# Kernel tuning notes

Hardware: AMD Instinct MI355X
Metric: run time of the kernel (lower is better)

## Reference

```python
import jax, jax.numpy as jnp
import numpy as np

N, K, DIN = 2, 2048, 1024
H, DOUT = 16, 64


def setup_inputs() -> dict:
    key = jax.random.key(0)
    ks = jax.random.split(key, 12)
    c_qk = float(np.sqrt(6.0 / (DIN + DOUT)))  # per-head q/k init scale
    c_v = c_qk  # dim_q == dim_v == DOUT here
    u = lambda k, shape, c: jax.random.uniform(k, shape, jnp.float32, -c, c)
    inp = {
        "query": jax.random.normal(ks[0], (N, K, DIN), jnp.float32),
        "key": jax.random.normal(ks[1], (N, K, DIN), jnp.float32),
        "value": jax.random.normal(ks[2], (N, K, DIN), jnp.float32),
        "mask": jax.random.randint(ks[3], (N, K, K), 0, 2) > 0,  # bool (N,K,K)
        # stacked per-head projection weights: (H, DIN, DOUT), biases (H, DOUT)
        "Wq": u(ks[4], (H, DIN, DOUT), c_qk),
        "bq": u(ks[5], (H, DOUT), c_qk),
        "Wk": u(ks[6], (H, DIN, DOUT), c_qk),
        "bk": u(ks[7], (H, DOUT), c_qk),
        "Wv": u(ks[8], (H, DIN, DOUT), c_v),
        "bv": u(ks[9], (H, DOUT), c_v),
        # output projection: (H*DOUT, DIN)
        "Wp": u(ks[10], (H * DOUT, DIN), c_qk),
        "bp": u(ks[11], (DIN,), c_qk),
    }
    return inp


def reference(query, key, value, mask, Wq, bq, Wk, bk, Wv, bv, Wp, bp):
    # Per-head projections, batched over heads: (N,K,DIN) x (H,DIN,DOUT) -> (N,H,K,DOUT)
    q = jnp.einsum("nkm,hmd->nhkd", query, Wq) + bq[None, :, None, :]
    k = jnp.einsum("nkm,hmd->nhkd", key, Wk) + bk[None, :, None, :]
    v = jnp.einsum("nkm,hmd->nhkd", value, Wv) + bv[None, :, None, :]
    # scaled dot-product scores: (N,H,K,K), scaled by sqrt(per-head dim)
    scores = jnp.einsum("nhkd,nhld->nhkl", q, k) / jnp.sqrt(jnp.asarray(DOUT, q.dtype))
    scores = jnp.where(mask[:, None, :, :], jnp.asarray(-1e9, scores.dtype), scores)
    w = jax.nn.softmax(scores, axis=-1)
    y = jnp.einsum("nhkl,nhld->nhkd", w, v)  # (N,H,K,DOUT)
    # concat heads along feature dim (head order matches torch cat over head list)
    y = jnp.transpose(y, (0, 2, 1, 3)).reshape(N, K, H * DOUT)
    return y @ Wp + bp
```

## Files before the change

kernel.cpp:

```cpp
#include <hip/hip_runtime.h>
#include <hip/hip_bf16.h>
#include <stdint.h>

typedef __attribute__((ext_vector_type(8))) __bf16 bf16x8;
typedef __attribute__((ext_vector_type(2))) __bf16 bf16x2;
typedef __attribute__((ext_vector_type(4))) float floatx4;

#define NB 2
#define SEQ 2048
#define DIN 1024
#define NH 16
#define DH 64
#define DMODEL 1024
#define BQ 128
#define BK 64
#define PAD 72
#define QSCALE 0.18033688011112042f

__device__ __forceinline__ float bf2f(unsigned short u) {
    return __uint_as_float(((unsigned)u) << 16);
}
__device__ __forceinline__ unsigned short f2bf(float f) {
    unsigned u = __float_as_uint(f);
    unsigned r = (u + 0x7FFFu + ((u >> 16) & 1u)) >> 16;
    return (unsigned short)r;
}
__device__ __forceinline__ float ldin(const void* p, size_t idx, int isbf) {
    return isbf ? bf2f(((const unsigned short*)p)[idx]) : ((const float*)p)[idx];
}

__device__ __forceinline__ void gl_lds16(const void* g, void* l) {
    __builtin_amdgcn_global_load_lds(
        reinterpret_cast<__attribute__((address_space(1))) unsigned int*>(
            reinterpret_cast<uintptr_t>(g)),
        reinterpret_cast<__attribute__((address_space(3))) unsigned int*>(
            reinterpret_cast<uintptr_t>(l)),
        16, 0, 0);
}

__device__ __forceinline__ int wave_is_bf16(const void* p) {
    unsigned short u = ((const unsigned short*)p)[2 * (threadIdx.x & 63)];
    int e = (u >> 7) & 0xFF;
    int sane = (u == 0 || (e > 100 && e < 140)) ? 1 : 0;
    return __popcll(__ballot(sane)) >= 32;
}
__device__ __forceinline__ int wave_mask_is_int(const void* p) {
    int v = ((const int*)p)[threadIdx.x & 63];
    int zo = (v == 0 || v == 1) ? 1 : 0;
    return __popcll(__ballot(zo)) >= 48;
}

__global__ __launch_bounds__(256) void prep(
    const void* __restrict__ q, const void* __restrict__ k, const void* __restrict__ v,
    const void* __restrict__ mask,
    const void* __restrict__ wq, const void* __restrict__ wk,
    const void* __restrict__ wv, const void* __restrict__ wp,
    unsigned short* __restrict__ a0, unsigned short* __restrict__ a1,
    unsigned short* __restrict__ a2,
    unsigned short* __restrict__ t0, unsigned short* __restrict__ t1,
    unsigned short* __restrict__ t2, unsigned short* __restrict__ t3,
    unsigned int* __restrict__ mbits)
{
    __shared__ float xls[64][68];
    const int b = blockIdx.x;
    const int tid = threadIdx.x;
    if (b < 12288) {
        int z = b >> 12, blk = b & 4095;
        const void* src = (z == 0) ? q : (z == 1) ? k : v;
        unsigned short* dst = (z == 0) ? a0 : (z == 1) ? a1 : a2;
        int isbf = wave_is_bf16(src);
        size_t i = ((size_t)blk * 256 + tid) * 4;
        if (isbf) {
            *(ushort4*)&dst[i] = *(const ushort4*)((const unsigned short*)src + i);
        } else {
            float4 f = *(const float4*)((const float*)src + i);
            ushort4 o;
            o.x = f2bf(f.x); o.y = f2bf(f.y); o.z = f2bf(f.z); o.w = f2bf(f.w);
            *(ushort4*)&dst[i] = o;
        }
    } else if (b < 13312) {
        int blk = b - 12288;
        int w = blk * 256 + tid;
        int is_int = wave_mask_is_int(mask);
        unsigned bits = 0;
        if (is_int) {
            const int4* p = (const int4*)mask + (size_t)w * 8;
#pragma unroll
            for (int g = 0; g < 8; ++g) {
                int4 vv = p[g];
                bits |= (unsigned)(vv.x != 0) << (g * 4 + 0);
                bits |= (unsigned)(vv.y != 0) << (g * 4 + 1);
                bits |= (unsigned)(vv.z != 0) << (g * 4 + 2);
                bits |= (unsigned)(vv.w != 0) << (g * 4 + 3);
            }
        } else {
            const uint4* p = (const uint4*)mask + (size_t)w * 2;
#pragma unroll
            for (int g = 0; g < 2; ++g) {
                uint4 vv = p[g];
                unsigned ws4[4] = {vv.x, vv.y, vv.z, vv.w};
#pragma unroll
                for (int c = 0; c < 4; ++c)
#pragma unroll
                    for (int bb = 0; bb < 4; ++bb)
                        bits |= (unsigned)(((ws4[c] >> (8 * bb)) & 0xFFu) != 0)
                                << (g * 16 + c * 4 + bb);
            }
        }
        mbits[w] = bits;
    } else {
        int zb = b - 13312;
        int z = zb >> 8, t = zb & 255;
        const void* src = (z == 0) ? wq : (z == 1) ? wk : (z == 2) ? wv : wp;
        unsigned short* dst = (z == 0) ? t0 : (z == 1) ? t1 : (z == 2) ? t2 : t3;
        int isbf = wave_is_bf16(src);
        int r = tid >> 2, cs = (tid & 3) * 16;
        if (z < 3) {
            int h = t >> 4, m0 = (t & 15) * 64;
#pragma unroll
            for (int j = 0; j < 16; ++j)
                xls[r][cs + j] = ldin(src, (size_t)h * 65536 + (size_t)(m0 + r) * 64 + cs + j, isbf);
            __syncthreads();
            int d2 = tid >> 2, ms = (tid & 3) * 16;
            size_t orow = (size_t)(h * 64 + d2) * 1024 + m0 + ms;
#pragma unroll
            for (int g = 0; g < 4; ++g) {
                ushort4 o;
                o.x = f2bf(xls[ms + g * 4 + 0][d2]);
                o.y = f2bf(xls[ms + g * 4 + 1][d2]);
                o.z = f2bf(xls[ms + g * 4 + 2][d2]);
                o.w = f2bf(xls[ms + g * 4 + 3][d2]);
                *(ushort4*)&dst[orow + g * 4] = o;
            }
        } else {
            int m0 = (t >> 4) * 64, c0 = (t & 15) * 64;
#pragma unroll
            for (int j = 0; j < 16; ++j)
                xls[r][cs + j] = ldin(src, (size_t)(m0 + r) * 1024 + c0 + cs + j, isbf);
            __syncthreads();
            int d2 = tid >> 2, ms = (tid & 3) * 16;
            size_t orow = (size_t)(c0 + d2) * 1024 + m0 + ms;
#pragma unroll
            for (int g = 0; g < 4; ++g) {
                ushort4 o;
                o.x = f2bf(xls[ms + g * 4 + 0][d2]);
                o.y = f2bf(xls[ms + g * 4 + 1][d2]);
                o.z = f2bf(xls[ms + g * 4 + 2][d2]);
                o.w = f2bf(xls[ms + g * 4 + 3][d2]);
                *(ushort4*)&dst[orow + g * 4] = o;
            }
        }
    }
}

__global__ __launch_bounds__(256) void expand_mask(
    const unsigned int* __restrict__ mbits, unsigned short* __restrict__ m16)
{
    int gid = blockIdx.x * 256 + threadIdx.x;
    unsigned w = mbits[gid];
    unsigned wrd[16];
#pragma unroll
    for (int i = 0; i < 16; ++i) {
        unsigned lo = ((w >> (2 * i)) & 1u) - 1u;
        unsigned hi = ((w >> (2 * i + 1)) & 1u) - 1u;
        wrd[i] = (lo & 0xFFFFu) | (hi << 16);
    }
    uint4* dst = (uint4*)&m16[(size_t)gid * 32];
#pragma unroll
    for (int g = 0; g < 4; ++g) dst[g] = *(uint4*)&wrd[g * 4];
}

__global__ __launch_bounds__(256) void gemm_mfma(
    const unsigned short* __restrict__ A0, const unsigned short* __restrict__ A1,
    const unsigned short* __restrict__ A2,
    const unsigned short* __restrict__ B0, const unsigned short* __restrict__ B1,
    const unsigned short* __restrict__ B2,
    const void* __restrict__ bias0, const void* __restrict__ bias1,
    const void* __restrict__ bias2,
    void* __restrict__ C0, void* __restrict__ C1, void* __restrict__ C2,
    int mode0)
{
    const int z = blockIdx.z;
    const unsigned short* A  = (z == 0) ? A0 : (z == 1) ? A1 : A2;
    const unsigned short* BT = (z == 0) ? B0 : (z == 1) ? B1 : B2;
    const void* bias = (z == 0) ? bias0 : (z == 1) ? bias1 : bias2;
    void* C = (z == 0) ? C0 : (z == 1) ? C1 : C2;
    const int mode = mode0 + z;
    const int isbf = wave_is_bf16(bias);
    const float scl = (mode == 0) ? QSCALE : 1.0f;

    const int n0  = blockIdx.x * 128;
    const int m0g = blockIdx.y * 128;
    const int tid = threadIdx.x;
    const int wave = tid >> 6, lane = tid & 63;
    const int l16 = lane & 15, quad = lane >> 4;
    const int wm = wave & 1, wn = wave >> 1;

    __shared__ __align__(16) unsigned short smem[17408];
    unsigned short* As = smem;
    unsigned short* Bs = smem + 8192;

    floatx4 acc[4][4];
#pragma unroll
    for (int mt = 0; mt < 4; ++mt)
#pragma unroll
        for (int nt = 0; nt < 4; ++nt) acc[mt][nt] = floatx4{0.f, 0.f, 0.f, 0.f};

    const int lrow8 = lane >> 3;
    const int lseg  = (lane & 7) * 8;

    for (int kk = 0; kk < 1024; kk += 64) {
#pragma unroll
        for (int j = 0; j < 4; ++j) {
            int row0 = wave * 8 + j * 32;
            gl_lds16(&A[(size_t)(m0g + row0 + lrow8) * 1024 + kk + lseg], &As[row0 * 64]);
            gl_lds16(&BT[(size_t)(n0 + row0 + lrow8) * 1024 + kk + lseg], &Bs[row0 * 64]);
        }
        __syncthreads();
#pragma unroll
        for (int ks = 0; ks < 2; ++ks) {
            bf16x8 af[4], bf[4];
#pragma unroll
            for (int mt = 0; mt < 4; ++mt)
                af[mt] = *(const bf16x8*)&As[(wm * 64 + mt * 16 + l16) * 64 + ks * 32 + quad * 8];
#pragma unroll
            for (int nt = 0; nt < 4; ++nt)
                bf[nt] = *(const bf16x8*)&Bs[(wn * 64 + nt * 16 + l16) * 64 + ks * 32 + quad * 8];
#pragma unroll
            for (int mt = 0; mt < 4; ++mt)
#pragma unroll
                for (int nt = 0; nt < 4; ++nt)
                    acc[mt][nt] = __builtin_amdgcn_mfma_f32_16x16x32_bf16(af[mt], bf[nt], acc[mt][nt], 0, 0, 0);
        }
        __syncthreads();
    }

    float bv4[4];
#pragma unroll
    for (int nt = 0; nt < 4; ++nt)
        bv4[nt] = ldin(bias, n0 + wn * 64 + nt * 16 + l16, isbf);

    if (mode <= 1) {
        unsigned short* O = (unsigned short*)C;
#pragma unroll
        for (int mt = 0; mt < 4; ++mt)
#pragma unroll
            for (int reg = 0; reg < 4; ++reg) {
                int row = m0g + wm * 64 + mt * 16 + quad * 4 + reg;
                int nb = row >> 11, kq = row & (SEQ - 1);
#pragma unroll
                for (int nt = 0; nt < 4; ++nt) {
                    int c = n0 + wn * 64 + nt * 16 + l16;
                    int h = c >> 6, d = c & 63;
                    O[(((size_t)nb * NH + h) * SEQ + kq) * DH + d] =
                        f2bf((acc[mt][nt][reg] + bv4[nt]) * scl);
                }
            }
    } else if (mode == 2) {
#pragma unroll
        for (int mt = 0; mt < 4; ++mt)
#pragma unroll
            for (int nt = 0; nt < 4; ++nt)
#pragma unroll
                for (int reg = 0; reg < 4; ++reg) {
                    int m_l = wm * 64 + mt * 16 + quad * 4 + reg;
                    int c_l = wn * 64 + nt * 16 + l16;
                    smem[c_l * 136 + m_l] = f2bf(acc[mt][nt][reg] + bv4[nt]);
                }
        __syncthreads();
        unsigned short* O = (unsigned short*)C;
        int nb = m0g >> 11;
        int kq0 = m0g & (SEQ - 1);
#pragma unroll
        for (int j = 0; j < 8; ++j) {
            int i = tid + j * 256;
            int c_l = i >> 4, m8 = (i & 15) * 8;
            int cg = n0 + c_l, h = cg >> 6, d = cg & 63;
            *(bf16x8*)&O[(((size_t)nb * NH + h) * DH + d) * SEQ + kq0 + m8] =
                *(const bf16x8*)&smem[c_l * 136 + m8];
        }
    } else {
        unsigned short* Ob = (unsigned short*)C;
        float* Of = (float*)C;
#pragma unroll
        for (int mt = 0; mt < 4; ++mt)
#pragma unroll
            for (int reg = 0; reg < 4; ++reg) {
                int row = m0g + wm * 64 + mt * 16 + quad * 4 + reg;
#pragma unroll
                for (int nt = 0; nt < 4; ++nt) {
                    int c = n0 + wn * 64 + nt * 16 + l16;
                    float v = acc[mt][nt][reg] + bv4[nt];
                    if (isbf) Ob[(size_t)row * DMODEL + c] = f2bf(v);
                    else      Of[(size_t)row * DMODEL + c] = v;
                }
            }
    }
}

__global__ __launch_bounds__(256, 2) void attn_mfma(
    const unsigned short* __restrict__ qws, const unsigned short* __restrict__ kws,
    const unsigned short* __restrict__ vtws, const unsigned short* __restrict__ m16,
    unsigned short* __restrict__ yws)
{
    const int qt   = blockIdx.x;
    const int h    = blockIdx.y;
    const int n    = blockIdx.z;
    const int tid  = threadIdx.x;
    const int wave = tid >> 6;
    const int lane = tid & 63;
    const int l16  = lane & 15;
    const int quad = lane >> 4;

    __shared__ __align__(16) unsigned short Ks[2][BK * DH];
    __shared__ __align__(16) unsigned short VTs[2][DH * BK];
    __shared__ __align__(16) unsigned short Ps[4][32 * PAD];

    const size_t base_nh = ((size_t)n * NH + h) * SEQ * DH;
    const size_t base_vt = ((size_t)n * NH + h) * DH * SEQ;
    const int q0 = qt * BQ;

    const unsigned short* mrl0;
    const unsigned short* mrl1;
    bf16x8 af[2][2];
    {
        int qr0 = q0 + wave * 32 + l16;
        int qr1 = qr0 + 16;
        mrl0 = m16 + ((size_t)n * SEQ + qr0) * SEQ;
        mrl1 = m16 + ((size_t)n * SEQ + qr1) * SEQ;
        const unsigned short* qp0 = qws + base_nh + (size_t)qr0 * DH + quad * 8;
        const unsigned short* qp1 = qws + base_nh + (size_t)qr1 * DH + quad * 8;
        af[0][0] = *(const bf16x8*)qp0;
        af[0][1] = *(const bf16x8*)(qp0 + 32);
        af[1][0] = *(const bf16x8*)qp1;
        af[1][1] = *(const bf16x8*)(qp1 + 32);
    }

    const int srow8  = lane >> 3;
    const int schunk = ((lane & 7) ^ srow8) * 8;
    const int swz = l16 & 7;
    int koff[2], voff[2];
#pragma unroll
    for (int ks = 0; ks < 2; ++ks) {
        koff[ks] = l16 * DH + (((ks * 4 + quad) ^ swz) * 8);
        voff[ks] = l16 * BK + (((ks * 4 + quad) ^ swz) * 8);
    }

    bf16x8 vones;
#pragma unroll
    for (int j = 0; j < 8; ++j) vones[j] = (__bf16)1.0f;

#pragma unroll
    for (int j = 0; j < 2; ++j) {
        int rl = wave * 16 + j * 8;
        gl_lds16(&kws[base_nh + (size_t)(rl + srow8) * DH + schunk], &Ks[0][rl * DH]);
        gl_lds16(&vtws[base_vt + (size_t)(rl + srow8) * SEQ + schunk], &VTs[0][rl * BK]);
    }

    floatx4 O[2][4];
#pragma unroll
    for (int g = 0; g < 2; ++g)
#pragma unroll
        for (int dt = 0; dt < 4; ++dt) O[g][dt] = floatx4{0.f, 0.f, 0.f, 0.f};
    floatx4 Lacc[2];
    Lacc[0] = floatx4{0.f, 0.f, 0.f, 0.f};
    Lacc[1] = floatx4{0.f, 0.f, 0.f, 0.f};

    __syncthreads();

    for (int it = 0; it < SEQ / BK; ++it) {
        const int cur = it & 1, nxt = cur ^ 1;
        const bool has_next = (it + 1) < (SEQ / BK);
        const int j0 = it * BK;
        const int j0n = j0 + BK;

        if (has_next) {
#pragma unroll
            for (int j = 0; j < 2; ++j) {
                int rl = wave * 16 + j * 8;
                gl_lds16(&kws[base_nh + (size_t)(j0n + rl + srow8) * DH + schunk], &Ks[nxt][rl * DH]);
                gl_lds16(&vtws[base_vt + (size_t)(rl + srow8) * SEQ + j0n + schunk], &VTs[nxt][rl * BK]);
            }
        }

        uint2 mm[2][4];
#pragma unroll
        for (int nt = 0; nt < 4; ++nt) {
            mm[0][nt] = *(const uint2*)&mrl0[j0 + nt * 16 + quad * 4];
            mm[1][nt] = *(const uint2*)&mrl1[j0 + nt * 16 + quad * 4];
        }

        bf16x8 bfK[4][2];
#pragma unroll
        for (int nt = 0; nt < 4; ++nt)
#pragma unroll
            for (int ks = 0; ks < 2; ++ks)
                bfK[nt][ks] = *(const bf16x8*)&Ks[cur][nt * 16 * DH + koff[ks]];

        float St[2][4][4];
#pragma unroll
        for (int nt = 0; nt < 4; ++nt) {
#pragma unroll
            for (int g = 0; g < 2; ++g) {
                floatx4 c = {0.f, 0.f, 0.f, 0.f};
                c = __builtin_amdgcn_mfma_f32_16x16x32_bf16(bfK[nt][0], af[g][0], c, 0, 0, 0);
                c = __builtin_amdgcn_mfma_f32_16x16x32_bf16(bfK[nt][1], af[g][1], c, 0, 0, 0);
                St[g][nt][0] = c[0]; St[g][nt][1] = c[1];
                St[g][nt][2] = c[2]; St[g][nt][3] = c[3];
            }
        }

#pragma unroll
        for (int g = 0; g < 2; ++g)
#pragma unroll
            for (int nt = 0; nt < 4; ++nt) {
                bf16x2 e01, e23;
                e01[0] = (__bf16)__builtin_amdgcn_exp2f(St[g][nt][0]);
                e01[1] = (__bf16)__builtin_amdgcn_exp2f(St[g][nt][1]);
                e23[0] = (__bf16)__builtin_amdgcn_exp2f(St[g][nt][2]);
                e23[1] = (__bf16)__builtin_amdgcn_exp2f(St[g][nt][3]);
                uint2 pk;
                pk.x = (*(unsigned*)&e01) & mm[g][nt].x;
                pk.y = (*(unsigned*)&e23) & mm[g][nt].y;
                *(uint2*)&Ps[wave][(g * 16 + l16) * PAD + nt * 16 + quad * 4] = pk;
            }

        bf16x8 pa[2][2], vb[4][2];
#pragma unroll
        for (int g = 0; g < 2; ++g)
#pragma unroll
            for (int ks = 0; ks < 2; ++ks)
                pa[g][ks] = *(const bf16x8*)&Ps[wave][(g * 16 + l16) * PAD + ks * 32 + quad * 8];
#pragma unroll
        for (int dt = 0; dt < 4; ++dt)
#pragma unroll
            for (int ks = 0; ks < 2; ++ks)
                vb[dt][ks] = *(const bf16x8*)&VTs[cur][dt * 16 * BK + voff[ks]];

        Lacc[0] = __builtin_amdgcn_mfma_f32_16x16x32_bf16(pa[0][0], vones, Lacc[0], 0, 0, 0);
        Lacc[1] = __builtin_amdgcn_mfma_f32_16x16x32_bf16(pa[1][0], vones, Lacc[1], 0, 0, 0);
        Lacc[0] = __builtin_amdgcn_mfma_f32_16x16x32_bf16(pa[0][1], vones, Lacc[0], 0, 0, 0);
        Lacc[1] = __builtin_amdgcn_mfma_f32_16x16x32_bf16(pa[1][1], vones, Lacc[1], 0, 0, 0);
#pragma unroll
        for (int dt = 0; dt < 4; ++dt) {
#pragma unroll
            for (int g = 0; g < 2; ++g) {
                O[g][dt] = __builtin_amdgcn_mfma_f32_16x16x32_bf16(pa[g][0], vb[dt][0], O[g][dt], 0, 0, 0);
                O[g][dt] = __builtin_amdgcn_mfma_f32_16x16x32_bf16(pa[g][1], vb[dt][1], O[g][dt], 0, 0, 0);
            }
        }

        __syncthreads();
    }

#pragma unroll
    for (int g = 0; g < 2; ++g)
#pragma unroll
        for (int r = 0; r < 4; ++r) {
            float lr = Lacc[g][r];
            float inv = (lr > 0.f) ? 1.f / lr : 0.f;
            int row = q0 + wave * 32 + g * 16 + quad * 4 + r;
#pragma unroll
            for (int dt = 0; dt < 4; ++dt) {
                int col = h * DH + dt * 16 + l16;
                yws[((size_t)n * SEQ + row) * DMODEL + col] = f2bf(O[g][dt][r] * inv);
            }
        }
}

extern "C" void kernel_launch(void* const* d_in, const int* in_sizes, int n_in,
                              void* d_out, int out_size, void* d_ws, size_t ws_size,
                              hipStream_t stream) {
    const void* query = d_in[0];
    const void* key_  = d_in[1];
    const void* value = d_in[2];
    const void* mask  = d_in[3];
    const void* Wq = d_in[4];
    const void* bq = d_in[5];
    const void* Wk = d_in[6];
    const void* bk = d_in[7];
    const void* Wv = d_in[8];
    const void* bv = d_in[9];
    const void* Wp = d_in[10];
    const void* bp = d_in[11];

    const size_t per = (size_t)NB * NH * SEQ * DH;
    unsigned short* us = (unsigned short*)d_ws;
    unsigned short* qws  = us;
    unsigned short* kws  = us + per;
    unsigned short* vtws = us + 2 * per;
    unsigned short* abf0 = us + 3 * per;
    unsigned short* abf1 = us + 4 * per;
    unsigned short* abf2 = us + 5 * per;
    unsigned short* wt0  = us + 6 * per;
    unsigned short* wt1  = wt0 + 1048576;
    unsigned short* wt2  = wt1 + 1048576;
    unsigned short* wt3  = wt2 + 1048576;
    unsigned int* mbits  = (unsigned int*)(wt3 + 1048576);
    unsigned short* yws = abf0;
    unsigned short* mask16 = abf1;

    prep<<<dim3(14336), 256, 0, stream>>>(query, key_, value, mask,
                                          Wq, Wk, Wv, Wp,
                                          abf0, abf1, abf2,
                                          wt0, wt1, wt2, wt3, mbits);
    gemm_mfma<<<dim3(8, 32, 3), 256, 0, stream>>>(abf0, abf1, abf2, wt0, wt1, wt2,
                                                  bq, bk, bv, qws, kws, vtws, 0);
    expand_mask<<<dim3(1024), 256, 0, stream>>>(mbits, mask16);
    attn_mfma<<<dim3(SEQ / BQ, NH, NB), 256, 0, stream>>>(qws, kws, vtws, mask16, yws);
    gemm_mfma<<<dim3(8, 32, 1), 256, 0, stream>>>(yws, yws, yws, wt3, wt3, wt3,
                                                  bp, bp, bp, d_out, d_out, d_out, 3);
}
```

Before: 310.8 us.

## Read packed mask bits directly in attention and remap blocks per XCD

```diff
diff --git a/kernel.cpp b/kernel.cpp
--- a/kernel.cpp
+++ b/kernel.cpp
@@ -153,23 +153,6 @@
     }
 }
 
-__global__ __launch_bounds__(256) void expand_mask(
-    const unsigned int* __restrict__ mbits, unsigned short* __restrict__ m16)
-{
-    int gid = blockIdx.x * 256 + threadIdx.x;
-    unsigned w = mbits[gid];
-    unsigned wrd[16];
-#pragma unroll
-    for (int i = 0; i < 16; ++i) {
-        unsigned lo = ((w >> (2 * i)) & 1u) - 1u;
-        unsigned hi = ((w >> (2 * i + 1)) & 1u) - 1u;
-        wrd[i] = (lo & 0xFFFFu) | (hi << 16);
-    }
-    uint4* dst = (uint4*)&m16[(size_t)gid * 32];
-#pragma unroll
-    for (int g = 0; g < 4; ++g) dst[g] = *(uint4*)&wrd[g * 4];
-}
-
 __global__ __launch_bounds__(256) void gemm_mfma(
     const unsigned short* __restrict__ A0, const unsigned short* __restrict__ A1,
     const unsigned short* __restrict__ A2,
@@ -300,12 +283,16 @@
 
 __global__ __launch_bounds__(256, 2) void attn_mfma(
     const unsigned short* __restrict__ qws, const unsigned short* __restrict__ kws,
-    const unsigned short* __restrict__ vtws, const unsigned short* __restrict__ m16,
+    const unsigned short* __restrict__ vtws, const unsigned int* __restrict__ mbits,
     unsigned short* __restrict__ yws)
 {
-    const int qt   = blockIdx.x;
-    const int h    = blockIdx.y;
-    const int n    = blockIdx.z;
+    const int linear = blockIdx.x + (blockIdx.y << 4) + (blockIdx.z << 8);
+    const int xcd = linear & 7, loc = linear >> 3;
+    const int hn  = (xcd << 2) + (loc >> 4);
+    const int qt  = loc & 15;
+    const int h   = hn & 15;
+    const int n   = hn >> 4;
+
     const int tid  = threadIdx.x;
     const int wave = tid >> 6;
     const int lane = tid & 63;
@@ -320,14 +307,14 @@
     const size_t base_vt = ((size_t)n * NH + h) * DH * SEQ;
     const int q0 = qt * BQ;
 
-    const unsigned short* mrl0;
-    const unsigned short* mrl1;
+    const unsigned int* mr0;
+    const unsigned int* mr1;
     bf16x8 af[2][2];
     {
         int qr0 = q0 + wave * 32 + l16;
         int qr1 = qr0 + 16;
-        mrl0 = m16 + ((size_t)n * SEQ + qr0) * SEQ;
-        mrl1 = m16 + ((size_t)n * SEQ + qr1) * SEQ;
+        mr0 = mbits + ((size_t)n * SEQ + qr0) * (SEQ / 32);
+        mr1 = mbits + ((size_t)n * SEQ + qr1) * (SEQ / 32);
         const unsigned short* qp0 = qws + base_nh + (size_t)qr0 * DH + quad * 8;
         const unsigned short* qp1 = qws + base_nh + (size_t)qr1 * DH + quad * 8;
         af[0][0] = *(const bf16x8*)qp0;
@@ -383,12 +370,8 @@
             }
         }
 
-        uint2 mm[2][4];
-#pragma unroll
-        for (int nt = 0; nt < 4; ++nt) {
-            mm[0][nt] = *(const uint2*)&mrl0[j0 + nt * 16 + quad * 4];
-            mm[1][nt] = *(const uint2*)&mrl1[j0 + nt * 16 + quad * 4];
-        }
+        uint2 mwA = *(const uint2*)&mr0[j0 >> 5];
+        uint2 mwB = *(const uint2*)&mr1[j0 >> 5];
 
         bf16x8 bfK[4][2];
 #pragma unroll
@@ -411,19 +394,27 @@
         }
 
 #pragma unroll
-        for (int g = 0; g < 2; ++g)
+        for (int g = 0; g < 2; ++g) {
+            uint2 mw = g ? mwB : mwA;
 #pragma unroll
             for (int nt = 0; nt < 4; ++nt) {
+                unsigned w = (nt & 2) ? mw.y : mw.x;
+                int bb = (nt & 1) * 16 + quad * 4;
+                float p[4];
+#pragma unroll
+                for (int r = 0; r < 4; ++r) {
+                    float e = __builtin_amdgcn_exp2f(St[g][nt][r]);
+                    p[r] = ((w >> (bb + r)) & 1u) ? 0.f : e;
+                }
                 bf16x2 e01, e23;
-                e01[0] = (__bf16)__builtin_amdgcn_exp2f(St[g][nt][0]);
-                e01[1] = (__bf16)__builtin_amdgcn_exp2f(St[g][nt][1]);
-                e23[0] = (__bf16)__builtin_amdgcn_exp2f(St[g][nt][2]);
-                e23[1] = (__bf16)__builtin_amdgcn_exp2f(St[g][nt][3]);
+                e01[0] = (__bf16)p[0]; e01[1] = (__bf16)p[1];
+                e23[0] = (__bf16)p[2]; e23[1] = (__bf16)p[3];
                 uint2 pk;
-                pk.x = (*(unsigned*)&e01) & mm[g][nt].x;
-                pk.y = (*(unsigned*)&e23) & mm[g][nt].y;
+                pk.x = *(unsigned*)&e01;
+                pk.y = *(unsigned*)&e23;
                 *(uint2*)&Ps[wave][(g * 16 + l16) * PAD + nt * 16 + quad * 4] = pk;
             }
+        }
 
         bf16x8 pa[2][2], vb[4][2];
 #pragma unroll
@@ -498,7 +489,6 @@
     unsigned short* wt3  = wt2 + 1048576;
     unsigned int* mbits  = (unsigned int*)(wt3 + 1048576);
     unsigned short* yws = abf0;
-    unsigned short* mask16 = abf1;
 
     prep<<<dim3(14336), 256, 0, stream>>>(query, key_, value, mask,
                                           Wq, Wk, Wv, Wp,
@@ -506,8 +496,7 @@
                                           wt0, wt1, wt2, wt3, mbits);
     gemm_mfma<<<dim3(8, 32, 3), 256, 0, stream>>>(abf0, abf1, abf2, wt0, wt1, wt2,
                                                   bq, bk, bv, qws, kws, vtws, 0);
-    expand_mask<<<dim3(1024), 256, 0, stream>>>(mbits, mask16);
-    attn_mfma<<<dim3(SEQ / BQ, NH, NB), 256, 0, stream>>>(qws, kws, vtws, mask16, yws);
+    attn_mfma<<<dim3(SEQ / BQ, NH, NB), 256, 0, stream>>>(qws, kws, vtws, mbits, yws);
     gemm_mfma<<<dim3(8, 32, 1), 256, 0, stream>>>(yws, yws, yws, wt3, wt3, wt3,
                                                   bp, bp, bp, d_out, d_out, d_out, 3);
 }
```

Result: faster. 287.8 us (-7.4%).
